# Optimization experiments

Hardware: AMD Instinct MI355X
Metric: run time of the kernel (lower is better)

Reference implementation:

```python
import jax, jax.numpy as jnp
import numpy as np

N_HEAD = 16
WINDOW = 256


def setup_inputs() -> dict:
    key = jax.random.key(0)
    ks = jax.random.split(key, 3)
    B, S, D = 2, 2048, 1024
    x = jax.random.normal(ks[0], (B, S, D), dtype=jnp.float32)
    w_attn = jax.random.normal(ks[1], (D, 3 * D), dtype=jnp.float32) * 0.02
    b_attn = jnp.zeros((3 * D,), dtype=jnp.float32)
    w_proj = jax.random.normal(ks[2], (D, D), dtype=jnp.float32) * 0.02
    b_proj = jnp.zeros((D,), dtype=jnp.float32)
    return {"x": x, "w_attn": w_attn, "b_attn": b_attn, "w_proj": w_proj, "b_proj": b_proj}


def reference(x, w_attn, b_attn, w_proj, b_proj):
    B, S, D = x.shape
    hd = D // N_HEAD  # head dim
    scale = 1.0 / np.sqrt(hd).astype(np.float32)

    # fused QKV projection (Conv1D == linear on last dim)
    c = jnp.einsum('bsd,df->bsf', x, w_attn) + b_attn
    q, k, v = jnp.split(c, 3, axis=-1)

    def split_heads(t):  # [B,S,D] -> [B,H,S,hd]
        return t.reshape(B, S, N_HEAD, hd).transpose(0, 2, 1, 3)

    q, k, v = split_heads(q), split_heads(k), split_heads(v)
    present = jnp.stack([k, v], axis=1)  # [B,2,H,S,hd]

    # scores [B,H,S,S]
    w = jnp.einsum('bhqd,bhkd->bhqk', q, k) * scale

    # causal sliding-window mask
    q_pos = jnp.arange(S)[:, None]
    k_pos = jnp.arange(S)[None, :]
    mask = (k_pos <= q_pos) & (k_pos >= q_pos - WINDOW + 1)  # [S,S]
    w = jnp.where(mask[None, None], w, jnp.finfo(w.dtype).min)
    w = jax.nn.softmax(w, axis=-1)

    a = jnp.einsum('bhqk,bhkd->bhqd', w, v)
    a = a.transpose(0, 2, 1, 3).reshape(B, S, D)  # merge heads
    out = jnp.einsum('bsd,df->bsf', a, w_proj) + b_proj
    return out, present
```

## Files before the change

kernel.cpp:

```cpp
#include <hip/hip_runtime.h>
#include <cstdint>
#include <cstddef>

typedef __bf16 bf16x8 __attribute__((ext_vector_type(8)));
typedef float f32x4 __attribute__((ext_vector_type(4)));

#define MFMA16(a, b, c) __builtin_amdgcn_mfma_f32_16x16x32_bf16(a, b, c, 0, 0, 0)

static __device__ __forceinline__ bf16x8 ld_bf16x8(const __bf16* p) {
    return *reinterpret_cast<const bf16x8*>(p);
}

static __device__ __forceinline__ void async_cp16(const __bf16* g, __bf16* l) {
    __builtin_amdgcn_global_load_lds((const __attribute__((address_space(1))) void*)g,
                                     (__attribute__((address_space(3))) void*)l, 16, 0, 0);
}

template <int N>
static __device__ __forceinline__ void wait_vmcnt() {
    asm volatile("s_waitcnt vmcnt(%0)" ::"n"(N) : "memory");
}

static __device__ __forceinline__ void barrier_pinned() {
    __builtin_amdgcn_sched_barrier(0);
    __builtin_amdgcn_s_barrier();
    __builtin_amdgcn_sched_barrier(0);
}

template <int CTRL>
static __device__ __forceinline__ float dppmv(float x) {
    return __builtin_bit_cast(float, __builtin_amdgcn_update_dpp(
        0, __builtin_bit_cast(int, x), CTRL, 0xF, 0xF, true));
}
static __device__ __forceinline__ float rmax16(float x) {
    x = fmaxf(x, dppmv<0x121>(x));
    x = fmaxf(x, dppmv<0x122>(x));
    x = fmaxf(x, dppmv<0x124>(x));
    x = fmaxf(x, dppmv<0x128>(x));
    return x;
}
static __device__ __forceinline__ float rsum16(float x) {
    x += dppmv<0x121>(x);
    x += dppmv<0x122>(x);
    x += dppmv<0x124>(x);
    x += dppmv<0x128>(x);
    return x;
}

__global__ void cvt_kernel(const float* __restrict__ src, __bf16* __restrict__ dst, int n8) {
    int i = blockIdx.x * blockDim.x + threadIdx.x;
    if (i >= n8) return;
    const float4* s4 = reinterpret_cast<const float4*>(src) + (size_t)i * 2;
    float4 a = s4[0], b = s4[1];
    bf16x8 o;
    o[0] = (__bf16)a.x; o[1] = (__bf16)a.y; o[2] = (__bf16)a.z; o[3] = (__bf16)a.w;
    o[4] = (__bf16)b.x; o[5] = (__bf16)b.y; o[6] = (__bf16)b.z; o[7] = (__bf16)b.w;
    reinterpret_cast<bf16x8*>(dst)[i] = o;
}

__global__ __launch_bounds__(256) void tcvt_kernel(const float* __restrict__ in,
                                                   __bf16* __restrict__ out, int K, int N) {
    __shared__ __bf16 T[64][72];
    const int k0 = blockIdx.y * 64, n0 = blockIdx.x * 64;
    const int t = threadIdx.x;
    const int col = (t & 15) << 2;
    const int rowb = t >> 4;
    #pragma unroll
    for (int i = 0; i < 4; i++) {
        int row = i * 16 + rowb;
        float4 v = *reinterpret_cast<const float4*>(&in[(size_t)(k0 + row) * N + n0 + col]);
        T[col + 0][row] = (__bf16)v.x;
        T[col + 1][row] = (__bf16)v.y;
        T[col + 2][row] = (__bf16)v.z;
        T[col + 3][row] = (__bf16)v.w;
    }
    __syncthreads();
    const int oc = (t & 7) << 3;
    const int orb = t >> 3;
    #pragma unroll
    for (int i = 0; i < 2; i++) {
        int r = i * 32 + orb;
        bf16x8 v = *reinterpret_cast<bf16x8*>(&T[r][oc]);
        *reinterpret_cast<bf16x8*>(&out[(size_t)(n0 + r) * K + k0 + oc]) = v;
    }
}

template <int BM, int BN, int WM, int WN>
__device__ __forceinline__ void mainloop2(const __bf16* __restrict__ A,
                                          const __bf16* __restrict__ Bt,
                                          int K, int row0, int col0,
                                          __bf16* lds,
                                          f32x4 (&acc)[BM / WM / 16][BN / WN / 16]) {
    constexpr int MR = BM / WM / 16, NR = BN / WN / 16;
    constexpr int AE = BM * 32;
    constexpr int BUFE = AE + BN * 32;
    constexpr int APW = BM / 16 / 8;
    constexpr int BPW = BN / 16 / 8;
    const int tid = threadIdx.x, l = tid & 63, w = tid >> 6;
    const int wm = w / WN, wn = w % WN;
    const int lr = l >> 2;
    const int lcs = (((l & 3) ^ ((l >> 3) & 3)) << 3);
    const int fr = l & 15;
    const int fc = (((l >> 4) ^ ((l >> 1) & 3)) << 3);

    const size_t arow = (size_t)(row0 + lr) * K + lcs;
    const size_t brow = (size_t)(col0 + lr) * K + lcs;
    const int nt = K >> 5;

    auto stage = [&](int t, int buf) {
        const int k0 = t << 5;
        const int bb = buf * BUFE;
        #pragma unroll
        for (int j = 0; j < APW; j++) {
            const int mi = w * APW + j;
            async_cp16(A + arow + (size_t)mi * 16 * K + k0, lds + bb + mi * 512 + l * 8);
        }
        #pragma unroll
        for (int j = 0; j < BPW; j++) {
            const int ni = w * BPW + j;
            async_cp16(Bt + brow + (size_t)ni * 16 * K + k0, lds + bb + AE + ni * 512 + l * 8);
        }
    };

    stage(0, 0);
    stage(1, 1);

    const int aoff = (wm * (BM / WM) + fr) * 32 + fc;
    const int boff = AE + (wn * (BN / WN) + fr) * 32 + fc;

    int p = 0;
    for (int t = 0; t < nt; ++t) {
        if (t + 1 < nt) {
            wait_vmcnt<APW + BPW>();
        } else {
            wait_vmcnt<0>();
        }
        barrier_pinned();
        if (t + 2 < nt) {
            int p2 = p + 2; if (p2 >= 3) p2 -= 3;
            stage(t + 2, p2);
        }
        const int cb = p * BUFE;
        bf16x8 af[MR], bfv[NR];
        #pragma unroll
        for (int m = 0; m < MR; m++) af[m] = ld_bf16x8(&lds[cb + aoff + m * 512]);
        #pragma unroll
        for (int n = 0; n < NR; n++) bfv[n] = ld_bf16x8(&lds[cb + boff + n * 512]);
        __builtin_amdgcn_s_setprio(1);
        #pragma unroll
        for (int m = 0; m < MR; m++) {
            #pragma unroll
            for (int n = 0; n < NR; n++) {
                acc[m][n] = MFMA16(af[m], bfv[n], acc[m][n]);
            }
        }
        __builtin_amdgcn_s_setprio(0);
        asm volatile("s_waitcnt lgkmcnt(0)" ::: "memory");
        __builtin_amdgcn_sched_barrier(0);
        p = (p == 2) ? 0 : p + 1;
    }
}

__global__ __launch_bounds__(512, 2) void gemm_qkv_kernel(const __bf16* __restrict__ xb,
                                                          const __bf16* __restrict__ wabt,
                                                          const float* __restrict__ bias,
                                                          __bf16* __restrict__ qb,
                                                          __bf16* __restrict__ kb,
                                                          __bf16* __restrict__ vt,
                                                          float* __restrict__ present) {
    __shared__ __bf16 lds[3 * (128 * 32 + 128 * 32)];
    f32x4 acc[2][4] = {};
    const int row0 = blockIdx.y * 128, col0 = blockIdx.x * 128;
    mainloop2<128, 128, 4, 2>(xb, wabt, 1024, row0, col0, lds, acc);

    const int l = threadIdx.x & 63, w = threadIdx.x >> 6;
    const int wm = w >> 1, wn = w & 1;
    const int part = col0 >> 10;
    #pragma unroll
    for (int n = 0; n < 4; n++) {
        int col = col0 + wn * 64 + n * 16 + (l & 15);
        int hh = (col >> 6) & 15;
        int dd = col & 63;
        float bv = bias[col];
        #pragma unroll
        for (int m = 0; m < 2; m++) {
            #pragma unroll
            for (int r = 0; r < 4; r++) {
                int row = row0 + wm * 32 + m * 16 + ((l >> 4) << 2) + r;
                int bb = row >> 11, ss = row & 2047;
                float val = acc[m][n][r] + bv;
                size_t qi = (((size_t)(bb * 16 + hh)) * 2048 + ss) * 64 + dd;
                if (part == 0) {
                    qb[qi] = (__bf16)val;
                } else if (part == 1) {
                    kb[qi] = (__bf16)val;
                    present[(((size_t)((bb * 2 + 0) * 16 + hh)) * 2048 + ss) * 64 + dd] = val;
                } else {
                    vt[(((size_t)(bb * 16 + hh)) * 64 + dd) * 2048 + ss] = (__bf16)val;
                    present[(((size_t)((bb * 2 + 1) * 16 + hh)) * 2048 + ss) * 64 + dd] = val;
                }
            }
        }
    }
}

__global__ __launch_bounds__(512, 2) void gemm_proj_kernel(const __bf16* __restrict__ ab,
                                                           const __bf16* __restrict__ wpbt,
                                                           const float* __restrict__ bias,
                                                           float* __restrict__ out) {
    __shared__ __bf16 lds[3 * (128 * 32 + 128 * 32)];
    f32x4 acc[2][4] = {};
    const int row0 = blockIdx.y * 128, col0 = blockIdx.x * 128;
    mainloop2<128, 128, 4, 2>(ab, wpbt, 1024, row0, col0, lds, acc);

    const int lane = threadIdx.x & 63, w = threadIdx.x >> 6;
    const int wm = w >> 1, wn = w & 1;
    #pragma unroll
    for (int n = 0; n < 4; n++) {
        int col = col0 + wn * 64 + n * 16 + (lane & 15);
        float bv = bias[col];
        #pragma unroll
        for (int m = 0; m < 2; m++) {
            #pragma unroll
            for (int r = 0; r < 4; r++) {
                int row = row0 + wm * 32 + m * 16 + ((lane >> 4) << 2) + r;
                out[(size_t)row * 1024 + col] = acc[m][n][r] + bv;
            }
        }
    }
}

__global__ __launch_bounds__(256) void attn_kernel(const __bf16* __restrict__ qb,
                                                   const __bf16* __restrict__ kb,
                                                   const __bf16* __restrict__ vtb,
                                                   __bf16* __restrict__ ab) {
    __shared__ __bf16 Pls[4][16 * 40];
    const int bh = blockIdx.x >> 5;
    const int qt = blockIdx.x & 31;
    const int lane = threadIdx.x & 63, wid = threadIdx.x >> 6;
    const int q0w = qt * 64 + wid * 16;

    const __bf16* Qh = qb + (size_t)bh * 2048 * 64;
    const __bf16* Kh = kb + (size_t)bh * 2048 * 64;
    const __bf16* Vt = vtb + (size_t)bh * 64 * 2048;
    __bf16* Pw = &Pls[wid][0];

    bf16x8 qf[2];
    {
        int qr = q0w + (lane & 15);
        const __bf16* qp = Qh + (size_t)qr * 64 + ((lane >> 4) << 3);
        qf[0] = ld_bf16x8(qp);
        qf[1] = ld_bf16x8(qp + 32);
    }

    f32x4 o[4];
    #pragma unroll
    for (int dt = 0; dt < 4; dt++) o[dt] = (f32x4){0.f, 0.f, 0.f, 0.f};
    float mrun[4] = {-1e30f, -1e30f, -1e30f, -1e30f};
    float srun[4] = {0.f, 0.f, 0.f, 0.f};

    const float cl2 = 0.18033688f;
    int klo = q0w - 255;
    int kt0 = klo > 0 ? (klo & ~31) : 0;

    for (int kt = kt0; kt <= q0w + 15; kt += 32) {
        bf16x8 vf[4];
        #pragma unroll
        for (int dt = 0; dt < 4; dt++)
            vf[dt] = ld_bf16x8(&Vt[(size_t)(dt * 16 + (lane & 15)) * 2048 + kt + ((lane >> 4) << 3)]);
        f32x4 s[2];
        #pragma unroll
        for (int kc = 0; kc < 2; kc++) {
            int krow = kt + kc * 16 + (lane & 15);
            const __bf16* kp = Kh + (size_t)krow * 64 + ((lane >> 4) << 3);
            bf16x8 kf0 = ld_bf16x8(kp);
            bf16x8 kf1 = ld_bf16x8(kp + 32);
            f32x4 a = (f32x4){0.f, 0.f, 0.f, 0.f};
            a = MFMA16(qf[0], kf0, a);
            a = MFMA16(qf[1], kf1, a);
            s[kc] = a;
        }
        const bool clean = (kt >= q0w - 240) && (kt + 31 <= q0w);
        float p0v[4], p1v[4];
        if (clean) {
            float s0v[4], s1v[4], mx[4];
            #pragma unroll
            for (int r = 0; r < 4; r++) {
                s0v[r] = s[0][r] * cl2;
                s1v[r] = s[1][r] * cl2;
                mx[r] = rmax16(fmaxf(s0v[r], s1v[r]));
            }
            float grow = fmaxf(fmaxf(mx[0] - mrun[0], mx[1] - mrun[1]),
                               fmaxf(mx[2] - mrun[2], mx[3] - mrun[3]));
            if (__all(grow <= 8.f)) {
                #pragma unroll
                for (int r = 0; r < 4; r++) {
                    float p0 = exp2f(s0v[r] - mrun[r]);
                    float p1 = exp2f(s1v[r] - mrun[r]);
                    srun[r] += rsum16(p0 + p1);
                    p0v[r] = p0;
                    p1v[r] = p1;
                }
            } else {
                float factor[4];
                #pragma unroll
                for (int r = 0; r < 4; r++) {
                    float mn = fmaxf(mrun[r], mx[r]);
                    float f = exp2f(mrun[r] - mn);
                    float p0 = exp2f(s0v[r] - mn);
                    float p1 = exp2f(s1v[r] - mn);
                    srun[r] = srun[r] * f + rsum16(p0 + p1);
                    mrun[r] = mn;
                    factor[r] = f;
                    p0v[r] = p0;
                    p1v[r] = p1;
                }
                #pragma unroll
                for (int dt = 0; dt < 4; dt++) {
                    #pragma unroll
                    for (int r = 0; r < 4; r++) o[dt][r] *= factor[r];
                }
            }
        } else {
            float factor[4];
            #pragma unroll
            for (int r = 0; r < 4; r++) {
                int q = q0w + ((lane >> 4) << 2) + r;
                int k0i = kt + (lane & 15);
                int k1i = k0i + 16;
                bool ok0 = (k0i <= q) && (k0i > q - 256);
                bool ok1 = (k1i <= q) && (k1i > q - 256);
                float s0 = ok0 ? s[0][r] * cl2 : -1e30f;
                float s1 = ok1 ? s[1][r] * cl2 : -1e30f;
                float mx = rmax16(fmaxf(s0, s1));
                float mn = fmaxf(mrun[r], mx);
                float f = exp2f(mrun[r] - mn);
                float p0 = ok0 ? exp2f(s0 - mn) : 0.f;
                float p1 = ok1 ? exp2f(s1 - mn) : 0.f;
                srun[r] = srun[r] * f + rsum16(p0 + p1);
                mrun[r] = mn;
                factor[r] = f;
                p0v[r] = p0;
                p1v[r] = p1;
            }
            #pragma unroll
            for (int dt = 0; dt < 4; dt++) {
                #pragma unroll
                for (int r = 0; r < 4; r++) o[dt][r] *= factor[r];
            }
        }
        #pragma unroll
        for (int r = 0; r < 4; r++) {
            int qrow = ((lane >> 4) << 2) + r;
            Pw[qrow * 40 + (lane & 15)] = (__bf16)p0v[r];
            Pw[qrow * 40 + 16 + (lane & 15)] = (__bf16)p1v[r];
        }
        asm volatile("s_waitcnt lgkmcnt(0)" ::: "memory");
        bf16x8 pf = ld_bf16x8(&Pw[(lane & 15) * 40 + ((lane >> 4) << 3)]);
        #pragma unroll
        for (int dt = 0; dt < 4; dt++) {
            o[dt] = MFMA16(pf, vf[dt], o[dt]);
        }
    }

    const int bb = bh >> 4, hh = bh & 15;
    #pragma unroll
    for (int r = 0; r < 4; r++) {
        int q = q0w + ((lane >> 4) << 2) + r;
        float inv = 1.f / srun[r];
        size_t base = ((size_t)bb * 2048 + q) * 1024 + hh * 64;
        #pragma unroll
        for (int dt = 0; dt < 4; dt++) {
            ab[base + dt * 16 + (lane & 15)] = (__bf16)(o[dt][r] * inv);
        }
    }
}

extern "C" void kernel_launch(void* const* d_in, const int* in_sizes, int n_in,
                              void* d_out, int out_size, void* d_ws, size_t ws_size,
                              hipStream_t stream) {
    const float* x = (const float*)d_in[0];
    const float* w_attn = (const float*)d_in[1];
    const float* b_attn = (const float*)d_in[2];
    const float* w_proj = (const float*)d_in[3];
    const float* b_proj = (const float*)d_in[4];

    float* out = (float*)d_out;
    float* present = out + (size_t)2 * 2048 * 1024;

    char* w = (char*)d_ws;
    __bf16* xb   = (__bf16*)(w);
    __bf16* wabt = (__bf16*)(w + 8388608);
    __bf16* wpbt = (__bf16*)(w + 14680064);
    __bf16* qb   = (__bf16*)(w + 16777216);
    __bf16* kb   = (__bf16*)(w + 25165824);
    __bf16* vt   = (__bf16*)(w + 33554432);
    __bf16* ab   = xb;

    cvt_kernel<<<2048, 256, 0, stream>>>(x, xb, 524288);
    tcvt_kernel<<<dim3(48, 16), 256, 0, stream>>>(w_attn, wabt, 1024, 3072);
    tcvt_kernel<<<dim3(16, 16), 256, 0, stream>>>(w_proj, wpbt, 1024, 1024);

    gemm_qkv_kernel<<<dim3(24, 32), 512, 0, stream>>>(xb, wabt, b_attn, qb, kb, vt, present);

    attn_kernel<<<1024, 256, 0, stream>>>(qb, kb, vt, ab);

    gemm_proj_kernel<<<dim3(8, 32), 512, 0, stream>>>(ab, wpbt, b_proj, out);
}
```

Before: 123.0 us.

## Enlarge QKV GEMM tile, widen attention key step to 64, remap blocks per XCD

The QKV GEMM moves to 256x128 tiles with half as many blocks, which raises per-block reuse at the cost of more LDS and accumulator registers. The attention kernel now handles 64 keys per iteration instead of 32, issues all K/V loads up front, and raises wave priority around the MFMA groups. It also switches to the raw exp2 builtin and moves the scale multiply after the row max in the clean path. Blocks are remapped so that consecutive heads land on the same XCD for L2 locality. The wider key step means more masked work in the edge tiles and higher register pressure.

Measured after the change: 125.9 us. 1.02x slower.

```diff
diff --git a/kernel.cpp b/kernel.cpp
--- a/kernel.cpp
+++ b/kernel.cpp
@@ -25,6 +25,10 @@
     __builtin_amdgcn_sched_barrier(0);
     __builtin_amdgcn_s_barrier();
     __builtin_amdgcn_sched_barrier(0);
+}
+
+static __device__ __forceinline__ float ex2(float x) {
+    return __builtin_amdgcn_exp2f(x);
 }
 
 template <int CTRL>
@@ -168,10 +172,10 @@
                                                           __bf16* __restrict__ kb,
                                                           __bf16* __restrict__ vt,
                                                           float* __restrict__ present) {
-    __shared__ __bf16 lds[3 * (128 * 32 + 128 * 32)];
-    f32x4 acc[2][4] = {};
-    const int row0 = blockIdx.y * 128, col0 = blockIdx.x * 128;
-    mainloop2<128, 128, 4, 2>(xb, wabt, 1024, row0, col0, lds, acc);
+    __shared__ __bf16 lds[3 * (256 * 32 + 128 * 32)];
+    f32x4 acc[4][4] = {};
+    const int row0 = blockIdx.y * 256, col0 = blockIdx.x * 128;
+    mainloop2<256, 128, 4, 2>(xb, wabt, 1024, row0, col0, lds, acc);
 
     const int l = threadIdx.x & 63, w = threadIdx.x >> 6;
     const int wm = w >> 1, wn = w & 1;
@@ -183,10 +187,10 @@
         int dd = col & 63;
         float bv = bias[col];
         #pragma unroll
-        for (int m = 0; m < 2; m++) {
+        for (int m = 0; m < 4; m++) {
             #pragma unroll
             for (int r = 0; r < 4; r++) {
-                int row = row0 + wm * 32 + m * 16 + ((l >> 4) << 2) + r;
+                int row = row0 + wm * 64 + m * 16 + ((l >> 4) << 2) + r;
                 int bb = row >> 11, ss = row & 2047;
                 float val = acc[m][n][r] + bv;
                 size_t qi = (((size_t)(bb * 16 + hh)) * 2048 + ss) * 64 + dd;
@@ -234,9 +238,11 @@
                                                    const __bf16* __restrict__ kb,
                                                    const __bf16* __restrict__ vtb,
                                                    __bf16* __restrict__ ab) {
-    __shared__ __bf16 Pls[4][16 * 40];
-    const int bh = blockIdx.x >> 5;
-    const int qt = blockIdx.x & 31;
+    __shared__ __bf16 Pls[4][16 * 72];
+    const int bidx = blockIdx.x;
+    const int xcd = bidx & 7, idx = bidx >> 3;
+    const int bh = (xcd << 2) | (idx & 3);
+    const int qt = idx >> 2;
     const int lane = threadIdx.x & 63, wid = threadIdx.x >> 6;
     const int q0w = qt * 64 + wid * 16;
 
@@ -245,10 +251,11 @@
     const __bf16* Vt = vtb + (size_t)bh * 64 * 2048;
     __bf16* Pw = &Pls[wid][0];
 
+    const int ld16 = lane & 15, hi3 = (lane >> 4) << 3;
+
     bf16x8 qf[2];
     {
-        int qr = q0w + (lane & 15);
-        const __bf16* qp = Qh + (size_t)qr * 64 + ((lane >> 4) << 3);
+        const __bf16* qp = Qh + (size_t)(q0w + ld16) * 64 + hi3;
         qf[0] = ld_bf16x8(qp);
         qf[1] = ld_bf16x8(qp + 32);
     }
@@ -261,59 +268,69 @@
 
     const float cl2 = 0.18033688f;
     int klo = q0w - 255;
-    int kt0 = klo > 0 ? (klo & ~31) : 0;
-
-    for (int kt = kt0; kt <= q0w + 15; kt += 32) {
-        bf16x8 vf[4];
-        #pragma unroll
-        for (int dt = 0; dt < 4; dt++)
-            vf[dt] = ld_bf16x8(&Vt[(size_t)(dt * 16 + (lane & 15)) * 2048 + kt + ((lane >> 4) << 3)]);
-        f32x4 s[2];
-        #pragma unroll
-        for (int kc = 0; kc < 2; kc++) {
-            int krow = kt + kc * 16 + (lane & 15);
-            const __bf16* kp = Kh + (size_t)krow * 64 + ((lane >> 4) << 3);
-            bf16x8 kf0 = ld_bf16x8(kp);
-            bf16x8 kf1 = ld_bf16x8(kp + 32);
+    int kt0 = klo > 0 ? (klo & ~63) : 0;
+    const int ktend = q0w + 15;
+
+    for (int kt = kt0; kt <= ktend; kt += 64) {
+        bf16x8 kf[4][2];
+        #pragma unroll
+        for (int kc = 0; kc < 4; kc++) {
+            const __bf16* kp = Kh + (size_t)(kt + kc * 16 + ld16) * 64 + hi3;
+            kf[kc][0] = ld_bf16x8(kp);
+            kf[kc][1] = ld_bf16x8(kp + 32);
+        }
+        bf16x8 va[4], vb[4];
+        #pragma unroll
+        for (int dt = 0; dt < 4; dt++) {
+            const __bf16* vp = &Vt[(size_t)(dt * 16 + ld16) * 2048 + kt + hi3];
+            va[dt] = ld_bf16x8(vp);
+            vb[dt] = ld_bf16x8(vp + 32);
+        }
+        f32x4 s[4];
+        __builtin_amdgcn_s_setprio(1);
+        #pragma unroll
+        for (int kc = 0; kc < 4; kc++) {
             f32x4 a = (f32x4){0.f, 0.f, 0.f, 0.f};
-            a = MFMA16(qf[0], kf0, a);
-            a = MFMA16(qf[1], kf1, a);
+            a = MFMA16(qf[0], kf[kc][0], a);
+            a = MFMA16(qf[1], kf[kc][1], a);
             s[kc] = a;
         }
-        const bool clean = (kt >= q0w - 240) && (kt + 31 <= q0w);
-        float p0v[4], p1v[4];
+        __builtin_amdgcn_s_setprio(0);
+        const bool clean = (kt >= q0w - 240) && (kt + 63 <= q0w);
+        float pv0[4], pv1[4], pv2[4], pv3[4];
         if (clean) {
-            float s0v[4], s1v[4], mx[4];
+            float mxs[4];
             #pragma unroll
             for (int r = 0; r < 4; r++) {
-                s0v[r] = s[0][r] * cl2;
-                s1v[r] = s[1][r] * cl2;
-                mx[r] = rmax16(fmaxf(s0v[r], s1v[r]));
-            }
-            float grow = fmaxf(fmaxf(mx[0] - mrun[0], mx[1] - mrun[1]),
-                               fmaxf(mx[2] - mrun[2], mx[3] - mrun[3]));
+                float m = fmaxf(fmaxf(s[0][r], s[1][r]), fmaxf(s[2][r], s[3][r]));
+                mxs[r] = rmax16(m) * cl2;
+            }
+            float grow = fmaxf(fmaxf(mxs[0] - mrun[0], mxs[1] - mrun[1]),
+                               fmaxf(mxs[2] - mrun[2], mxs[3] - mrun[3]));
             if (__all(grow <= 8.f)) {
                 #pragma unroll
                 for (int r = 0; r < 4; r++) {
-                    float p0 = exp2f(s0v[r] - mrun[r]);
-                    float p1 = exp2f(s1v[r] - mrun[r]);
-                    srun[r] += rsum16(p0 + p1);
-                    p0v[r] = p0;
-                    p1v[r] = p1;
+                    float p0 = ex2(s[0][r] * cl2 - mrun[r]);
+                    float p1 = ex2(s[1][r] * cl2 - mrun[r]);
+                    float p2 = ex2(s[2][r] * cl2 - mrun[r]);
+                    float p3 = ex2(s[3][r] * cl2 - mrun[r]);
+                    srun[r] += rsum16((p0 + p1) + (p2 + p3));
+                    pv0[r] = p0; pv1[r] = p1; pv2[r] = p2; pv3[r] = p3;
                 }
             } else {
                 float factor[4];
                 #pragma unroll
                 for (int r = 0; r < 4; r++) {
-                    float mn = fmaxf(mrun[r], mx[r]);
-                    float f = exp2f(mrun[r] - mn);
-                    float p0 = exp2f(s0v[r] - mn);
-                    float p1 = exp2f(s1v[r] - mn);
-                    srun[r] = srun[r] * f + rsum16(p0 + p1);
+                    float mn = fmaxf(mrun[r], mxs[r]);
+                    float f = ex2(mrun[r] - mn);
+                    float p0 = ex2(s[0][r] * cl2 - mn);
+                    float p1 = ex2(s[1][r] * cl2 - mn);
+                    float p2 = ex2(s[2][r] * cl2 - mn);
+                    float p3 = ex2(s[3][r] * cl2 - mn);
+                    srun[r] = srun[r] * f + rsum16((p0 + p1) + (p2 + p3));
                     mrun[r] = mn;
                     factor[r] = f;
-                    p0v[r] = p0;
-                    p1v[r] = p1;
+                    pv0[r] = p0; pv1[r] = p1; pv2[r] = p2; pv3[r] = p3;
                 }
                 #pragma unroll
                 for (int dt = 0; dt < 4; dt++) {
@@ -326,22 +343,26 @@
             #pragma unroll
             for (int r = 0; r < 4; r++) {
                 int q = q0w + ((lane >> 4) << 2) + r;
-                int k0i = kt + (lane & 15);
-                int k1i = k0i + 16;
-                bool ok0 = (k0i <= q) && (k0i > q - 256);
-                bool ok1 = (k1i <= q) && (k1i > q - 256);
-                float s0 = ok0 ? s[0][r] * cl2 : -1e30f;
-                float s1 = ok1 ? s[1][r] * cl2 : -1e30f;
-                float mx = rmax16(fmaxf(s0, s1));
+                int kb0 = kt + ld16;
+                bool ok0 = (kb0 <= q) && (kb0 > q - 256);
+                bool ok1 = (kb0 + 16 <= q) && (kb0 + 16 > q - 256);
+                bool ok2 = (kb0 + 32 <= q) && (kb0 + 32 > q - 256);
+                bool ok3 = (kb0 + 48 <= q) && (kb0 + 48 > q - 256);
+                float t0 = ok0 ? s[0][r] * cl2 : -1e30f;
+                float t1 = ok1 ? s[1][r] * cl2 : -1e30f;
+                float t2 = ok2 ? s[2][r] * cl2 : -1e30f;
+                float t3 = ok3 ? s[3][r] * cl2 : -1e30f;
+                float mx = rmax16(fmaxf(fmaxf(t0, t1), fmaxf(t2, t3)));
                 float mn = fmaxf(mrun[r], mx);
-                float f = exp2f(mrun[r] - mn);
-                float p0 = ok0 ? exp2f(s0 - mn) : 0.f;
-                float p1 = ok1 ? exp2f(s1 - mn) : 0.f;
-                srun[r] = srun[r] * f + rsum16(p0 + p1);
+                float f = ex2(mrun[r] - mn);
+                float p0 = ok0 ? ex2(t0 - mn) : 0.f;
+                float p1 = ok1 ? ex2(t1 - mn) : 0.f;
+                float p2 = ok2 ? ex2(t2 - mn) : 0.f;
+                float p3 = ok3 ? ex2(t3 - mn) : 0.f;
+                srun[r] = srun[r] * f + rsum16((p0 + p1) + (p2 + p3));
                 mrun[r] = mn;
                 factor[r] = f;
-                p0v[r] = p0;
-                p1v[r] = p1;
+                pv0[r] = p0; pv1[r] = p1; pv2[r] = p2; pv3[r] = p3;
             }
             #pragma unroll
             for (int dt = 0; dt < 4; dt++) {
@@ -352,15 +373,20 @@
         #pragma unroll
         for (int r = 0; r < 4; r++) {
             int qrow = ((lane >> 4) << 2) + r;
-            Pw[qrow * 40 + (lane & 15)] = (__bf16)p0v[r];
-            Pw[qrow * 40 + 16 + (lane & 15)] = (__bf16)p1v[r];
+            Pw[qrow * 72 + ld16]      = (__bf16)pv0[r];
+            Pw[qrow * 72 + 16 + ld16] = (__bf16)pv1[r];
+            Pw[qrow * 72 + 32 + ld16] = (__bf16)pv2[r];
+            Pw[qrow * 72 + 48 + ld16] = (__bf16)pv3[r];
         }
         asm volatile("s_waitcnt lgkmcnt(0)" ::: "memory");
-        bf16x8 pf = ld_bf16x8(&Pw[(lane & 15) * 40 + ((lane >> 4) << 3)]);
-        #pragma unroll
-        for (int dt = 0; dt < 4; dt++) {
-            o[dt] = MFMA16(pf, vf[dt], o[dt]);
-        }
+        bf16x8 pfA = ld_bf16x8(&Pw[ld16 * 72 + hi3]);
+        bf16x8 pfB = ld_bf16x8(&Pw[ld16 * 72 + 32 + hi3]);
+        __builtin_amdgcn_s_setprio(1);
+        #pragma unroll
+        for (int dt = 0; dt < 4; dt++) o[dt] = MFMA16(pfA, va[dt], o[dt]);
+        #pragma unroll
+        for (int dt = 0; dt < 4; dt++) o[dt] = MFMA16(pfB, vb[dt], o[dt]);
+        __builtin_amdgcn_s_setprio(0);
     }
 
     const int bb = bh >> 4, hh = bh & 15;
@@ -371,7 +397,7 @@
         size_t base = ((size_t)bb * 2048 + q) * 1024 + hh * 64;
         #pragma unroll
         for (int dt = 0; dt < 4; dt++) {
-            ab[base + dt * 16 + (lane & 15)] = (__bf16)(o[dt][r] * inv);
+            ab[base + dt * 16 + ld16] = (__bf16)(o[dt][r] * inv);
         }
     }
 }
@@ -401,7 +427,7 @@
     tcvt_kernel<<<dim3(48, 16), 256, 0, stream>>>(w_attn, wabt, 1024, 3072);
     tcvt_kernel<<<dim3(16, 16), 256, 0, stream>>>(w_proj, wpbt, 1024, 1024);
 
-    gemm_qkv_kernel<<<dim3(24, 32), 512, 0, stream>>>(xb, wabt, b_attn, qb, kb, vt, present);
+    gemm_qkv_kernel<<<dim3(24, 16), 512, 0, stream>>>(xb, wabt, b_attn, qb, kb, vt, present);
 
     attn_kernel<<<1024, 256, 0, stream>>>(qb, kb, vt, ab);
 
```
